# Kernel tuning notes

Hardware: AMD Instinct MI355X
Metric: run time of the kernel (lower is better)

Reference implementation:

```python
import jax, jax.numpy as jnp
import numpy as np

SHIFTS = [1, 3, 5, 7]
C = 16  # in_channels // 4
# -1 neighbor offsets for tmp1..tmp8 (dy, dx) in units of the dilation
OFFSETS = [(-1, -1), (-1, 0), (-1, 1), (0, 1), (1, 1), (1, 0), (1, -1), (0, -1)]


def setup_inputs() -> dict:
    key = jax.random.key(0)
    ks = jax.random.split(key, 32)
    d = {}
    d['cen'] = jax.random.normal(ks[0], (8, 64, 256, 256), jnp.float32)
    d['mas'] = jax.random.normal(ks[1], (8, 1, 256, 256), jnp.float32)
    d['in_conv_w'] = jax.random.normal(ks[2], (16, 64), jnp.float32) * 0.1
    d['in_conv_b'] = jax.random.normal(ks[3], (16,), jnp.float32) * 0.1
    for i, s in enumerate(SHIFTS):
        d[f'dw_w{s}'] = jax.random.normal(ks[4 + 2 * i], (16, 1, s, s), jnp.float32) * 0.1
        d[f'dw_b{s}'] = jax.random.normal(ks[5 + 2 * i], (16,), jnp.float32) * 0.1
    d['l1_w'] = jax.random.normal(ks[12], (4, 16, 4), jnp.float32) * 0.1
    d['l1_b'] = jax.random.normal(ks[13], (4, 16), jnp.float32) * 0.1
    d['l2_w'] = jax.random.normal(ks[14], (4, 16, 8), jnp.float32) * 0.1
    d['l2_b'] = jax.random.normal(ks[15], (4, 16), jnp.float32) * 0.1
    d['base_w'] = jax.random.normal(ks[16], (16, 4), jnp.float32) * 0.1
    d['bn_scale'] = jnp.ones((16,), jnp.float32)
    d['bn_bias'] = jnp.zeros((16,), jnp.float32)
    d['final_w'] = jax.random.normal(ks[17], (1, 16), jnp.float32) * 0.1
    d['final_b'] = jax.random.normal(ks[18], (1,), jnp.float32) * 0.1
    return d


def _dw_conv(x, w, b, pad):
    # depthwise conv, groups == channels
    y = jax.lax.conv_general_dilated(
        x, w, window_strides=(1, 1), padding=[(pad, pad), (pad, pad)],
        dimension_numbers=('NCHW', 'OIHW', 'NCHW'), feature_group_count=x.shape[1])
    return y + b[None, :, None, None]


def _shifted(x, dy, dx, d):
    # zero-padded shift: out(y,x) = in(y+dy, x+dx)
    H, W = x.shape[2], x.shape[3]
    p = jnp.pad(x, ((0, 0), (0, 0), (d, d), (d, d)))
    return p[:, :, d + dy:d + dy + H, d + dx:d + dx + W]


def _circ_shift(x, dw_w, dw_b, w1, b1, w2, b2, shift):
    x = _dw_conv(x, dw_w, dw_b, shift // 2)
    # tmp_k = x - x shifted by the k-th neighbor offset (dilation = shift)
    T = [x - _shifted(x, dy * shift, dx * shift, shift) for dy, dx in OFFSETS]
    # paired sums: S[k] = tmp_{k+1} + tmp_{k+5} (S repeats with period 4)
    S = [T[k] + T[k + 4] for k in range(4)]
    outs = []
    for k in range(8):  # fixed small structural loop
        feats = jnp.stack([S[(k + 1) % 4], S[(k + 3) % 4], S[(k + 2) % 4],
                           2.0 * T[(k + 4) % 8]], axis=2)  # (B,C,4,H,W)
        # grouped 1x1 conv (groups=C, 4C->C) == per-channel contraction over feature axis
        o = jnp.einsum('bcfhw,cf->bchw', feats, w1) + b1[None, :, None, None]
        outs.append(o * T[k])
    O = jnp.sort(jnp.stack(outs, axis=2), axis=2)  # (B,C,8,H,W) sorted over branch axis
    return jnp.einsum('bcfhw,cf->bchw', O, w2) + b2[None, :, None, None]


def reference(cen, mas, in_conv_w, in_conv_b, dw_w1, dw_b1, dw_w3, dw_b3,
              dw_w5, dw_b5, dw_w7, dw_b7, l1_w, l1_b, l2_w, l2_b,
              base_w, bn_scale, bn_bias, final_w, final_b):
    # in_conv: 1x1, in_channels -> C
    x = jnp.einsum('bihw,oi->bohw', cen, in_conv_w) + in_conv_b[None, :, None, None]
    dws = [(dw_w1, dw_b1), (dw_w3, dw_b3), (dw_w5, dw_b5), (dw_w7, dw_b7)]
    branches = [
        _circ_shift(x, dws[i][0], dws[i][1], l1_w[i], l1_b[i], l2_w[i], l2_b[i], SHIFTS[i])
        for i in range(len(SHIFTS))
    ]
    A = jnp.sort(jnp.stack(branches, axis=2), axis=2)  # (B,C,4,H,W)
    # out_conv: grouped 1x1 BaseConv (conv no-bias + BN(affine) + SiLU), then 1x1 -> 1, sigmoid
    y = jnp.einsum('bcfhw,cf->bchw', A, base_w)
    y = jax.nn.silu(y * bn_scale[None, :, None, None] + bn_bias[None, :, None, None])
    y = jnp.einsum('bchw,oc->bohw', y, final_w) + final_b[None, :, None, None]
    return jax.nn.sigmoid(y)
```

## Files before the change

kernel.cpp:

```cpp
#include <hip/hip_runtime.h>
#include <hip/hip_fp16.h>
#include <math.h>

#define HW 65536
#define PITCH 272
#define PLANE (PITCH * PITCH)

typedef float v2f __attribute__((ext_vector_type(2), aligned(8)));
typedef _Float16 h2 __attribute__((ext_vector_type(2)));

__device__ __forceinline__ h2 uh(unsigned u) { return __builtin_bit_cast(h2, u); }

#define CEH(a, b) { h2 _t = __builtin_elementwise_min(a, b); \
                    b = __builtin_elementwise_max(a, b); a = _t; }

__device__ __forceinline__ void sort8_h2(h2* v) {
    CEH(v[0], v[1]); CEH(v[2], v[3]); CEH(v[4], v[5]); CEH(v[6], v[7]);
    CEH(v[0], v[2]); CEH(v[1], v[3]); CEH(v[4], v[6]); CEH(v[5], v[7]);
    CEH(v[1], v[2]); CEH(v[5], v[6]); CEH(v[0], v[4]); CEH(v[3], v[7]);
    CEH(v[1], v[5]); CEH(v[2], v[6]);
    CEH(v[1], v[4]); CEH(v[3], v[6]);
    CEH(v[2], v[4]); CEH(v[3], v[5]);
    CEH(v[3], v[4]);
}
__device__ __forceinline__ void sort4_h2(h2* v) {
    CEH(v[0], v[1]); CEH(v[2], v[3]); CEH(v[0], v[2]); CEH(v[1], v[3]); CEH(v[1], v[2]);
}

__global__ __launch_bounds__(256) void k_pack(const float* __restrict__ l1w,
                                              const float* __restrict__ l1b,
                                              const float* __restrict__ l2w,
                                              const float* __restrict__ l2b,
                                              const float* __restrict__ bw,
                                              unsigned* __restrict__ wtab) {
    for (int t = threadIdx.x; t < 1088; t += 256) {
        float v = 0.f;
        if (t < 1024) {
            int c = t >> 6, i = (t >> 4) & 3, j = t & 15;
            if (j < 3)        v = l1w[i * 64 + c * 4 + j];
            else if (j == 3)  v = 2.f * l1w[i * 64 + c * 4 + 3];
            else if (j == 4)  v = l1b[i * 16 + c];
            else if (j < 13)  v = l2w[i * 128 + c * 8 + (j - 5)];
            else if (j == 13) v = l2b[i * 16 + c];
        } else {
            v = bw[t - 1024];
        }
        unsigned hs = (unsigned)__half_as_ushort(__float2half(v));
        wtab[t] = hs * 0x10001u;
    }
}

__global__ __launch_bounds__(256, 4) void k_inconv(const float* __restrict__ cen,
                                                   const float* __restrict__ w,
                                                   const float* __restrict__ bias,
                                                   __half* __restrict__ xh) {
    __shared__ float wl[1040];
    int tid = threadIdx.x;
    for (int t = tid; t < 1024; t += 256) wl[t] = w[(t & 15) * 64 + (t >> 4)];
    if (tid < 16) wl[1024 + tid] = bias[tid];
    __syncthreads();

    int q  = blockIdx.x * 256 + tid;
    int b_ = q >> 14;
    int hw = (q & 16383) * 4;
    const float* src = cen + (size_t)(b_ * 64) * HW + hw;

    float4 acc[16];
#pragma unroll
    for (int o = 0; o < 16; o++) { float bv = wl[1024 + o]; acc[o] = make_float4(bv, bv, bv, bv); }

#pragma unroll 4
    for (int i = 0; i < 64; i++) {
        float4 xv = *(const float4*)(src + (size_t)i * HW);
        const float4* wq = (const float4*)&wl[i * 16];
#pragma unroll
        for (int g = 0; g < 4; g++) {
            float4 f = wq[g];
            acc[g * 4 + 0].x += xv.x * f.x; acc[g * 4 + 0].y += xv.y * f.x;
            acc[g * 4 + 0].z += xv.z * f.x; acc[g * 4 + 0].w += xv.w * f.x;
            acc[g * 4 + 1].x += xv.x * f.y; acc[g * 4 + 1].y += xv.y * f.y;
            acc[g * 4 + 1].z += xv.z * f.y; acc[g * 4 + 1].w += xv.w * f.y;
            acc[g * 4 + 2].x += xv.x * f.z; acc[g * 4 + 2].y += xv.y * f.z;
            acc[g * 4 + 2].z += xv.z * f.z; acc[g * 4 + 2].w += xv.w * f.z;
            acc[g * 4 + 3].x += xv.x * f.w; acc[g * 4 + 3].y += xv.y * f.w;
            acc[g * 4 + 3].z += xv.z * f.w; acc[g * 4 + 3].w += xv.w * f.w;
        }
    }
    __half* dst = xh + (size_t)(b_ * 16) * HW + hw;
#pragma unroll
    for (int o = 0; o < 16; o++) {
        uint2 pk;
        pk.x = __builtin_bit_cast(unsigned, __floats2half2_rn(acc[o].x, acc[o].y));
        pk.y = __builtin_bit_cast(unsigned, __floats2half2_rn(acc[o].z, acc[o].w));
        *(uint2*)(dst + (size_t)o * HW) = pk;
    }
}

__global__ __launch_bounds__(256) void k_dw(const __half* __restrict__ xh,
    const float* __restrict__ dw_w1, const float* __restrict__ dw_b1,
    const float* __restrict__ dw_w3, const float* __restrict__ dw_b3,
    const float* __restrict__ dw_w5, const float* __restrict__ dw_b5,
    const float* __restrict__ dw_w7, const float* __restrict__ dw_b7,
    __half* __restrict__ conv) {
    const int plane = blockIdx.y;
    const int c     = plane & 15;
    const int P0    = (blockIdx.x >> 3) * 34;
    const int Q0    = (blockIdx.x & 7) * 34;
    const int tid   = threadIdx.x;

    __shared__ float lx[40 * 44];
    const __half* xp = xh + (size_t)plane * HW;

    for (int t = tid; t < 40 * 21; t += 256) {
        int r = t / 21, d = t - r * 21;
        int gy = P0 - 10 + r, gx = Q0 - 10 + 2 * d;
        float2 v = make_float2(0.f, 0.f);
        if ((unsigned)gy < 256u && (unsigned)gx < 256u)
            v = __half22float2(*(const __half2*)(xp + gy * 256 + gx));
        lx[r * 44 + 2 * d]     = v.x;
        lx[r * 44 + 2 * d + 1] = v.y;
    }
    __syncthreads();

    const float* W7 = dw_w7 + c * 49;
    const float* W5 = dw_w5 + c * 25;
    const float* W3 = dw_w3 + c * 9;
    const float  W1 = dw_w1[c];
    const float  B1 = dw_b1[c], B3 = dw_b3[c], B5 = dw_b5[c], B7 = dw_b7[c];

    for (int u = tid; u < 34 * 17; u += 256) {
        int row = u / 17;
        int pc0 = (u - row * 17) * 2;
        v2f c7v = {0, 0}, c5v = {0, 0}, c3v = {0, 0}, c1v = {0, 0};
#pragma unroll
        for (int a = 0; a < 7; a++) {
            const float* rp = &lx[(row + a) * 44 + pc0];
            v2f q0 = *(const v2f*)rp;
            v2f q1 = *(const v2f*)(rp + 2);
            v2f q2 = *(const v2f*)(rp + 4);
            v2f q3 = *(const v2f*)(rp + 6);
            float v8 = rp[8];
            float v[9] = {q0.x, q0.y, q1.x, q1.y, q2.x, q2.y, q3.x, q3.y, v8};
#pragma unroll
            for (int bb = 0; bb < 7; bb++) {
                v2f vv = {v[bb], v[bb + 1]};
                c7v += vv * W7[a * 7 + bb];
            }
            if (a >= 1 && a <= 5) {
#pragma unroll
                for (int bb = 0; bb < 5; bb++) {
                    v2f vv = {v[bb + 1], v[bb + 2]};
                    c5v += vv * W5[(a - 1) * 5 + bb];
                }
            }
            if (a >= 2 && a <= 4) {
#pragma unroll
                for (int bb = 0; bb < 3; bb++) {
                    v2f vv = {v[bb + 2], v[bb + 3]};
                    c3v += vv * W3[(a - 2) * 3 + bb];
                }
            }
            if (a == 3) {
                v2f vv = {v[3], v[4]};
                c1v = vv * W1;
            }
        }
        int py = P0 + row, px = Q0 + pc0;
        int iy = py - 7, ix = px - 7;
        bool rin = (unsigned)iy < 256u;
        bool in0 = rin && (unsigned)ix < 256u;
        bool in1 = rin && (unsigned)(ix + 1) < 256u;
        size_t o = (size_t)(plane * 4) * PLANE + (size_t)py * PITCH + px;
        *(__half2*)&conv[o]             = __floats2half2_rn(in0 ? c1v.x + B1 : 0.f, in1 ? c1v.y + B1 : 0.f);
        *(__half2*)&conv[o + PLANE]     = __floats2half2_rn(in0 ? c3v.x + B3 : 0.f, in1 ? c3v.y + B3 : 0.f);
        *(__half2*)&conv[o + 2 * PLANE] = __floats2half2_rn(in0 ? c5v.x + B5 : 0.f, in1 ? c5v.y + B5 : 0.f);
        *(__half2*)&conv[o + 3 * PLANE] = __floats2half2_rn(in0 ? c7v.x + B7 : 0.f, in1 ? c7v.y + B7 : 0.f);
    }
}

__global__ __launch_bounds__(512, 4) void k_mach(const __half* __restrict__ conv,
                                                 const unsigned* __restrict__ wtab,
                                                 const float* __restrict__ bns,
                                                 const float* __restrict__ bnb,
                                                 __half* __restrict__ y16) {
    const int by  = blockIdx.y;
    const int c   = by & 15;
    const int ty0 = (blockIdx.x >> 3) * 32;
    const int tx0 = (blockIdx.x & 7) * 32;
    const int tid = threadIdx.x;
    const int py  = tid >> 4;
    const int pxp = tid & 15;

    __shared__ __align__(16) unsigned convt[4 * 46 * 24];

    {
        const size_t pb4 = (size_t)(by * 4) * PLANE;
#pragma unroll
        for (int j = 0; j < 3; j++) {
            int t = tid + j * 512;
            if (t < 1104) {
                int i  = t / 276;
                int rm = t - i * 276;
                int r  = rm / 6;
                int d4 = rm - r * 6;
                size_t E = pb4 + (size_t)i * PLANE + (size_t)(ty0 + r) * PITCH + tx0 + 8 * d4;
                ((uint4*)convt)[t] = *(const uint4*)(conv + E);
            }
        }
    }
    __syncthreads();

    h2 bh[4];
#pragma unroll
    for (int i = 0; i < 4; i++) {
        const int s = 1 + 2 * i;
        const unsigned* pl = convt + i * 1104;
        const int q    = pxp + (7 - s) / 2;
        const int topb = (py + 7 - s) * 24 + q;
        const int midb = (py + 7) * 24 + q;
        const int botb = (py + 7 + s) * 24 + q;

        unsigned tt[8], tm[8], tb[8];
#pragma unroll
        for (int k = 0; k <= s; k++) {
            tt[k] = pl[topb + k];
            tm[k] = pl[midb + k];
            tb[k] = pl[botb + k];
        }
        const int m = s >> 1;
        h2 n0  = uh(tt[0]);
        h2 n1  = uh((tt[m] >> 16) | (tt[m + 1] << 16));
        h2 n2  = uh(tt[s]);
        h2 n7  = uh(tm[0]);
        h2 ctr = uh((tm[m] >> 16) | (tm[m + 1] << 16));
        h2 n3  = uh(tm[s]);
        h2 n6  = uh(tb[0]);
        h2 n5  = uh((tb[m] >> 16) | (tb[m + 1] << 16));
        h2 n4  = uh(tb[s]);

        h2 T[8];
        T[0] = ctr - n0; T[1] = ctr - n1; T[2] = ctr - n2; T[3] = ctr - n3;
        T[4] = ctr - n4; T[5] = ctr - n5; T[6] = ctr - n6; T[7] = ctr - n7;
        h2 S[4];
#pragma unroll
        for (int k = 0; k < 4; k++) S[k] = T[k] + T[k + 4];

        const unsigned* wt = wtab + ((c << 2) + i) * 16;
        h2 w10 = uh(wt[0]), w11 = uh(wt[1]), w12 = uh(wt[2]);
        h2 w13x2 = uh(wt[3]), bb1 = uh(wt[4]);

        h2 R[4];
#pragma unroll
        for (int mm = 0; mm < 4; mm++) {
            h2 r = S[(mm + 2) & 3] * w12 + bb1;
            r = S[(mm + 3) & 3] * w11 + r;
            r = S[(mm + 1) & 3] * w10 + r;
            R[mm] = r;
        }
        h2 h8[8];
#pragma unroll
        for (int k = 0; k < 8; k++)
            h8[k] = (T[(k + 4) & 7] * w13x2 + R[k & 3]) * T[k];
        sort8_h2(h8);

        h2 acc = uh(wt[13]);
#pragma unroll
        for (int k = 0; k < 8; k++) acc += h8[k] * uh(wt[5 + k]);
        bh[i] = acc;
    }
    sort4_h2(bh);
    h2 yv = bh[0] * uh(wtab[1024 + (c << 2)]);
#pragma unroll
    for (int k = 1; k < 4; k++) yv = bh[k] * uh(wtab[1024 + (c << 2) + k]) + yv;

    const float bsc = bns[c], bbi = bnb[c];
    float zx = fmaf((float)yv.x, bsc, bbi);
    float zy = fmaf((float)yv.y, bsc, bbi);
    float sx = zx / (1.f + __expf(-zx));
    float sy = zy / (1.f + __expf(-zy));
    *(__half2*)&y16[(size_t)by * HW + (ty0 + py) * 256 + tx0 + 2 * pxp] =
        __floats2half2_rn(sx, sy);
}

__global__ __launch_bounds__(256) void k_final(const __half* __restrict__ y16,
                                               const float* __restrict__ fw,
                                               const float* __restrict__ fb,
                                               float* __restrict__ out) {
    long t  = (long)blockIdx.x * 256 + threadIdx.x;
    long p0 = t * 2;
    int  b  = (int)(p0 >> 16);
    int  hw = (int)(p0 & 65535);

    float accx = fb[0], accy = fb[0];
#pragma unroll
    for (int cc = 0; cc < 16; cc++) {
        __half2 h = *(const __half2*)(y16 + (size_t)(b * 16 + cc) * HW + hw);
        float2 v = __half22float2(h);
        float wv = fw[cc];
        accx = fmaf(v.x, wv, accx);
        accy = fmaf(v.y, wv, accy);
    }
    float2 r;
    r.x = 1.f / (1.f + __expf(-accx));
    r.y = 1.f / (1.f + __expf(-accy));
    *(float2*)(out + p0) = r;
}

extern "C" void kernel_launch(void* const* d_in, const int* in_sizes, int n_in,
                              void* d_out, int out_size, void* d_ws, size_t ws_size,
                              hipStream_t stream) {
    (void)in_sizes; (void)n_in; (void)out_size; (void)ws_size;
    const float* cen   = (const float*)d_in[0];
    const float* in_w  = (const float*)d_in[2];
    const float* in_b  = (const float*)d_in[3];
    const float* dw_w1 = (const float*)d_in[4];
    const float* dw_b1 = (const float*)d_in[5];
    const float* dw_w3 = (const float*)d_in[6];
    const float* dw_b3 = (const float*)d_in[7];
    const float* dw_w5 = (const float*)d_in[8];
    const float* dw_b5 = (const float*)d_in[9];
    const float* dw_w7 = (const float*)d_in[10];
    const float* dw_b7 = (const float*)d_in[11];
    const float* l1w   = (const float*)d_in[12];
    const float* l1b   = (const float*)d_in[13];
    const float* l2w   = (const float*)d_in[14];
    const float* l2b   = (const float*)d_in[15];
    const float* bw    = (const float*)d_in[16];
    const float* bns   = (const float*)d_in[17];
    const float* bnb   = (const float*)d_in[18];
    const float* fw    = (const float*)d_in[19];
    const float* fb    = (const float*)d_in[20];

    __half*   xh   = (__half*)d_ws;
    __half*   conv = (__half*)((char*)d_ws + (size_t)16777216);
    unsigned* wtab = (unsigned*)((char*)d_ws + (size_t)16777216 + (size_t)75759616);
    __half*   y16  = (__half*)((char*)d_ws + (size_t)16777216 + (size_t)75759616 + 8192);
    float*    out  = (float*)d_out;

    k_pack<<<1, 256, 0, stream>>>(l1w, l1b, l2w, l2b, bw, wtab);
    k_inconv<<<512, 256, 0, stream>>>(cen, in_w, in_b, xh);
    k_dw<<<dim3(64, 128), 256, 0, stream>>>(xh, dw_w1, dw_b1, dw_w3, dw_b3,
                                            dw_w5, dw_b5, dw_w7, dw_b7, conv);
    k_mach<<<dim3(64, 128), 512, 0, stream>>>(conv, wtab, bns, bnb, y16);
    k_final<<<1024, 256, 0, stream>>>(y16, fw, fb, out);
}
```

Before: 364.8 us.

## Fuse depthwise convolutions into the shift/sort kernel via shared-memory tiles

Merges k_dw into k_mach so each block computes the four depthwise convolutions for its 32x32 tile plus a 7-pixel halo straight into shared memory. This drops the padded fp16 conv intermediate (about 75 MB written and then read back) and one kernel launch. The cost is recomputing the halo region for every tile (46x46 instead of 32x32) and heavier shared-memory use per block, which may reduce occupancy.

```diff
diff --git a/kernel.cpp b/kernel.cpp
--- a/kernel.cpp
+++ b/kernel.cpp
@@ -3,8 +3,6 @@
 #include <math.h>
 
 #define HW 65536
-#define PITCH 272
-#define PLANE (PITCH * PITCH)
 
 typedef float v2f __attribute__((ext_vector_type(2), aligned(8)));
 typedef _Float16 h2 __attribute__((ext_vector_type(2)));
@@ -96,119 +94,105 @@
     }
 }
 
-__global__ __launch_bounds__(256) void k_dw(const __half* __restrict__ xh,
+__global__ __launch_bounds__(512, 4) void k_fused(const __half* __restrict__ xh,
     const float* __restrict__ dw_w1, const float* __restrict__ dw_b1,
     const float* __restrict__ dw_w3, const float* __restrict__ dw_b3,
     const float* __restrict__ dw_w5, const float* __restrict__ dw_b5,
     const float* __restrict__ dw_w7, const float* __restrict__ dw_b7,
-    __half* __restrict__ conv) {
-    const int plane = blockIdx.y;
-    const int c     = plane & 15;
-    const int P0    = (blockIdx.x >> 3) * 34;
-    const int Q0    = (blockIdx.x & 7) * 34;
-    const int tid   = threadIdx.x;
-
-    __shared__ float lx[40 * 44];
-    const __half* xp = xh + (size_t)plane * HW;
-
-    for (int t = tid; t < 40 * 21; t += 256) {
-        int r = t / 21, d = t - r * 21;
-        int gy = P0 - 10 + r, gx = Q0 - 10 + 2 * d;
-        float2 v = make_float2(0.f, 0.f);
-        if ((unsigned)gy < 256u && (unsigned)gx < 256u)
-            v = __half22float2(*(const __half2*)(xp + gy * 256 + gx));
-        lx[r * 44 + 2 * d]     = v.x;
-        lx[r * 44 + 2 * d + 1] = v.y;
-    }
-    __syncthreads();
-
-    const float* W7 = dw_w7 + c * 49;
-    const float* W5 = dw_w5 + c * 25;
-    const float* W3 = dw_w3 + c * 9;
-    const float  W1 = dw_w1[c];
-    const float  B1 = dw_b1[c], B3 = dw_b3[c], B5 = dw_b5[c], B7 = dw_b7[c];
-
-    for (int u = tid; u < 34 * 17; u += 256) {
-        int row = u / 17;
-        int pc0 = (u - row * 17) * 2;
-        v2f c7v = {0, 0}, c5v = {0, 0}, c3v = {0, 0}, c1v = {0, 0};
-#pragma unroll
-        for (int a = 0; a < 7; a++) {
-            const float* rp = &lx[(row + a) * 44 + pc0];
-            v2f q0 = *(const v2f*)rp;
-            v2f q1 = *(const v2f*)(rp + 2);
-            v2f q2 = *(const v2f*)(rp + 4);
-            v2f q3 = *(const v2f*)(rp + 6);
-            float v8 = rp[8];
-            float v[9] = {q0.x, q0.y, q1.x, q1.y, q2.x, q2.y, q3.x, q3.y, v8};
-#pragma unroll
-            for (int bb = 0; bb < 7; bb++) {
-                v2f vv = {v[bb], v[bb + 1]};
-                c7v += vv * W7[a * 7 + bb];
-            }
-            if (a >= 1 && a <= 5) {
-#pragma unroll
-                for (int bb = 0; bb < 5; bb++) {
-                    v2f vv = {v[bb + 1], v[bb + 2]};
-                    c5v += vv * W5[(a - 1) * 5 + bb];
-                }
-            }
-            if (a >= 2 && a <= 4) {
-#pragma unroll
-                for (int bb = 0; bb < 3; bb++) {
-                    v2f vv = {v[bb + 2], v[bb + 3]};
-                    c3v += vv * W3[(a - 2) * 3 + bb];
-                }
-            }
-            if (a == 3) {
-                v2f vv = {v[3], v[4]};
-                c1v = vv * W1;
-            }
-        }
-        int py = P0 + row, px = Q0 + pc0;
-        int iy = py - 7, ix = px - 7;
-        bool rin = (unsigned)iy < 256u;
-        bool in0 = rin && (unsigned)ix < 256u;
-        bool in1 = rin && (unsigned)(ix + 1) < 256u;
-        size_t o = (size_t)(plane * 4) * PLANE + (size_t)py * PITCH + px;
-        *(__half2*)&conv[o]             = __floats2half2_rn(in0 ? c1v.x + B1 : 0.f, in1 ? c1v.y + B1 : 0.f);
-        *(__half2*)&conv[o + PLANE]     = __floats2half2_rn(in0 ? c3v.x + B3 : 0.f, in1 ? c3v.y + B3 : 0.f);
-        *(__half2*)&conv[o + 2 * PLANE] = __floats2half2_rn(in0 ? c5v.x + B5 : 0.f, in1 ? c5v.y + B5 : 0.f);
-        *(__half2*)&conv[o + 3 * PLANE] = __floats2half2_rn(in0 ? c7v.x + B7 : 0.f, in1 ? c7v.y + B7 : 0.f);
-    }
-}
-
-__global__ __launch_bounds__(512, 4) void k_mach(const __half* __restrict__ conv,
-                                                 const unsigned* __restrict__ wtab,
-                                                 const float* __restrict__ bns,
-                                                 const float* __restrict__ bnb,
-                                                 __half* __restrict__ y16) {
+    const unsigned* __restrict__ wtab,
+    const float* __restrict__ bns, const float* __restrict__ bnb,
+    __half* __restrict__ y16) {
+
     const int by  = blockIdx.y;
     const int c   = by & 15;
     const int ty0 = (blockIdx.x >> 3) * 32;
     const int tx0 = (blockIdx.x & 7) * 32;
     const int tid = threadIdx.x;
+
+    __shared__ float lx[52 * 56];
+    __shared__ __align__(16) unsigned convt[4 * 46 * 24];
+
+    const __half* xp = xh + (size_t)by * HW;
+    for (int t = tid; t < 676; t += 512) {
+        int r = t / 13, d = t - r * 13;
+        int gy = ty0 - 10 + r, gx0 = tx0 - 10 + 4 * d;
+        float a0 = 0.f, a1 = 0.f, a2 = 0.f, a3 = 0.f;
+        if ((unsigned)gy < 256u) {
+            const __half* rp = xp + gy * 256;
+            if (gx0 >= 0 && gx0 <= 252) {
+                uint2 u = *(const uint2*)(rp + gx0);
+                float2 f0 = __half22float2(__builtin_bit_cast(__half2, u.x));
+                float2 f1 = __half22float2(__builtin_bit_cast(__half2, u.y));
+                a0 = f0.x; a1 = f0.y; a2 = f1.x; a3 = f1.y;
+            } else {
+                if ((unsigned)(gx0 + 0) < 256u) a0 = __half2float(rp[gx0 + 0]);
+                if ((unsigned)(gx0 + 1) < 256u) a1 = __half2float(rp[gx0 + 1]);
+                if ((unsigned)(gx0 + 2) < 256u) a2 = __half2float(rp[gx0 + 2]);
+                if ((unsigned)(gx0 + 3) < 256u) a3 = __half2float(rp[gx0 + 3]);
+            }
+        }
+        *(float4*)&lx[r * 56 + 4 * d] = make_float4(a0, a1, a2, a3);
+    }
+    __syncthreads();
+
+    {
+        const float* W7 = dw_w7 + c * 49;
+        const float* W5 = dw_w5 + c * 25;
+        const float* W3 = dw_w3 + c * 9;
+        const float  W1 = dw_w1[c];
+        const float  B1 = dw_b1[c], B3 = dw_b3[c], B5 = dw_b5[c], B7 = dw_b7[c];
+
+        for (int u = tid; u < 46 * 23; u += 512) {
+            int row = u / 23;
+            int pc0 = (u - row * 23) * 2;
+            v2f c7v = {0, 0}, c5v = {0, 0}, c3v = {0, 0}, c1v = {0, 0};
+#pragma unroll
+            for (int a = 0; a < 7; a++) {
+                const float* rp = &lx[(row + a) * 56 + pc0];
+                v2f q0 = *(const v2f*)rp;
+                v2f q1 = *(const v2f*)(rp + 2);
+                v2f q2 = *(const v2f*)(rp + 4);
+                v2f q3 = *(const v2f*)(rp + 6);
+                float v[8] = {q0.x, q0.y, q1.x, q1.y, q2.x, q2.y, q3.x, q3.y};
+#pragma unroll
+                for (int bb = 0; bb < 7; bb++) {
+                    v2f vv = {v[bb], v[bb + 1]};
+                    c7v += vv * W7[a * 7 + bb];
+                }
+                if (a >= 1 && a <= 5) {
+#pragma unroll
+                    for (int bb = 0; bb < 5; bb++) {
+                        v2f vv = {v[bb + 1], v[bb + 2]};
+                        c5v += vv * W5[(a - 1) * 5 + bb];
+                    }
+                }
+                if (a >= 2 && a <= 4) {
+#pragma unroll
+                    for (int bb = 0; bb < 3; bb++) {
+                        v2f vv = {v[bb + 2], v[bb + 3]};
+                        c3v += vv * W3[(a - 2) * 3 + bb];
+                    }
+                }
+                if (a == 3) {
+                    v2f vv = {v[3], v[4]};
+                    c1v = vv * W1;
+                }
+            }
+            int iy = ty0 - 7 + row, ix = tx0 - 7 + pc0;
+            bool rin = (unsigned)iy < 256u;
+            bool in0 = rin && (unsigned)ix < 256u;
+            bool in1 = rin && (unsigned)(ix + 1) < 256u;
+            int o = row * 24 + (pc0 >> 1);
+            convt[o]        = __builtin_bit_cast(unsigned, __floats2half2_rn(in0 ? c1v.x + B1 : 0.f, in1 ? c1v.y + B1 : 0.f));
+            convt[o + 1104] = __builtin_bit_cast(unsigned, __floats2half2_rn(in0 ? c3v.x + B3 : 0.f, in1 ? c3v.y + B3 : 0.f));
+            convt[o + 2208] = __builtin_bit_cast(unsigned, __floats2half2_rn(in0 ? c5v.x + B5 : 0.f, in1 ? c5v.y + B5 : 0.f));
+            convt[o + 3312] = __builtin_bit_cast(unsigned, __floats2half2_rn(in0 ? c7v.x + B7 : 0.f, in1 ? c7v.y + B7 : 0.f));
+        }
+    }
+    __syncthreads();
+
     const int py  = tid >> 4;
     const int pxp = tid & 15;
-
-    __shared__ __align__(16) unsigned convt[4 * 46 * 24];
-
-    {
-        const size_t pb4 = (size_t)(by * 4) * PLANE;
-#pragma unroll
-        for (int j = 0; j < 3; j++) {
-            int t = tid + j * 512;
-            if (t < 1104) {
-                int i  = t / 276;
-                int rm = t - i * 276;
-                int r  = rm / 6;
-                int d4 = rm - r * 6;
-                size_t E = pb4 + (size_t)i * PLANE + (size_t)(ty0 + r) * PITCH + tx0 + 8 * d4;
-                ((uint4*)convt)[t] = *(const uint4*)(conv + E);
-            }
-        }
-    }
-    __syncthreads();
 
     h2 bh[4];
 #pragma unroll
@@ -332,15 +316,14 @@
     const float* fb    = (const float*)d_in[20];
 
     __half*   xh   = (__half*)d_ws;
-    __half*   conv = (__half*)((char*)d_ws + (size_t)16777216);
-    unsigned* wtab = (unsigned*)((char*)d_ws + (size_t)16777216 + (size_t)75759616);
-    __half*   y16  = (__half*)((char*)d_ws + (size_t)16777216 + (size_t)75759616 + 8192);
+    unsigned* wtab = (unsigned*)((char*)d_ws + (size_t)16777216);
+    __half*   y16  = (__half*)((char*)d_ws + (size_t)16777216 + 8192);
     float*    out  = (float*)d_out;
 
     k_pack<<<1, 256, 0, stream>>>(l1w, l1b, l2w, l2b, bw, wtab);
     k_inconv<<<512, 256, 0, stream>>>(cen, in_w, in_b, xh);
-    k_dw<<<dim3(64, 128), 256, 0, stream>>>(xh, dw_w1, dw_b1, dw_w3, dw_b3,
-                                            dw_w5, dw_b5, dw_w7, dw_b7, conv);
-    k_mach<<<dim3(64, 128), 512, 0, stream>>>(conv, wtab, bns, bnb, y16);
+    k_fused<<<dim3(64, 128), 512, 0, stream>>>(xh, dw_w1, dw_b1, dw_w3, dw_b3,
+                                               dw_w5, dw_b5, dw_w7, dw_b7,
+                                               wtab, bns, bnb, y16);
     k_final<<<1024, 256, 0, stream>>>(y16, fw, fb, out);
 }
```

Result: slower. 375.3 us (+2.9%).
